# Kernel optimization log

Measured on AMD Instinct MI355X. Metric: run time of the kernel, lower is better.

The kernel has to match this reference:

```python
import jax, jax.numpy as jnp
import numpy as np

FEA, DK, H = 512, 64, 8
B, L = 4, 2048
EPS = 1e-5


def _layernorm(x, g, b):
    mu = jnp.mean(x, axis=-1, keepdims=True)
    var = jnp.mean(jnp.square(x - mu), axis=-1, keepdims=True)
    return (x - mu) * jax.lax.rsqrt(var + EPS) * g + b


def setup_inputs() -> dict:
    key = jax.random.key(0)
    ks = jax.random.split(key, 12)
    d = {
        'qx': jax.random.normal(ks[0], (B, L, FEA), jnp.float32),
        'kx': jax.random.normal(ks[1], (B, L, FEA), jnp.float32),
        'vx': jax.random.normal(ks[2], (B, L, FEA), jnp.float32),
        'maskPAD': jax.random.randint(ks[3], (B, L, L), 0, 2, jnp.int32),
        # attention projections (stored as [in, out]); biases zero-init as in module
        'wq': jax.random.normal(ks[4], (FEA, DK * H), jnp.float32) * 0.02,
        'bq': jnp.zeros((DK * H,), jnp.float32),
        'wk': jax.random.normal(ks[5], (FEA, DK * H), jnp.float32) * 0.02,
        'bk': jnp.zeros((DK * H,), jnp.float32),
        'wv': jax.random.normal(ks[6], (FEA, DK * H), jnp.float32) * 0.02,
        'bv': jnp.zeros((DK * H,), jnp.float32),
        'wo': jax.random.normal(ks[7], (DK * H, FEA), jnp.float32) * 0.02,
        'bo': jnp.zeros((FEA,), jnp.float32),
        # FFN
        'w1': jax.random.normal(ks[8], (FEA, 4 * FEA), jnp.float32) * 0.02,
        'b1': jnp.zeros((4 * FEA,), jnp.float32),
        'w2': jax.random.normal(ks[9], (4 * FEA, FEA), jnp.float32) * 0.02,
        'b2': jnp.zeros((FEA,), jnp.float32),
        # layer norms
        'ln1_g': jnp.ones((FEA,), jnp.float32),
        'ln1_b': jnp.zeros((FEA,), jnp.float32),
        'ln2_g': jnp.ones((FEA,), jnp.float32),
        'ln2_b': jnp.zeros((FEA,), jnp.float32),
    }
    return d


def reference(qx, kx, vx, maskPAD, wq, bq, wk, bk, wv, bv, wo, bo,
              w1, b1, w2, b2, ln1_g, ln1_b, ln2_g, ln2_b):
    b, l, _ = qx.shape
    # project and split heads: [B, H, L, DK]
    q = (qx @ wq + bq).reshape(b, l, H, DK).transpose(0, 2, 1, 3)
    k = (kx @ wk + bk).reshape(b, l, H, DK).transpose(0, 2, 1, 3)
    v = (vx @ wv + bv).reshape(b, l, H, DK).transpose(0, 2, 1, 3)
    scores = jnp.einsum('bhqd,bhkd->bhqk', q, k) / np.sqrt(DK)  # [B,H,L,L]
    mask = (maskPAD == 0)[:, None, :, :]
    scores = jnp.where(mask, jnp.float32(-2 ** 15 + 1), scores)
    alpha = jax.nn.softmax(scores, axis=-1)
    z = jnp.einsum('bhqk,bhkd->bhqd', alpha, v)  # [B,H,L,DK]
    z = z.transpose(0, 2, 1, 3).reshape(b, l, H * DK)
    z = z @ wo + bo
    # post-LN FFN block (dropout = identity at inference)
    zn = _layernorm(vx + z, ln1_g, ln1_b)
    ffn = jax.nn.gelu(zn @ w1 + b1, approximate=False) @ w2 + b2
    return _layernorm(zn + ffn, ln2_g, ln2_b)
```

## Files before the change

kernel.cpp:

```cpp
#include <hip/hip_runtime.h>
#include <cstdint>


typedef __bf16 bf16;
typedef __bf16 bf16x8 __attribute__((ext_vector_type(8)));
typedef __bf16 bf16x2 __attribute__((ext_vector_type(2)));
typedef float floatx4 __attribute__((ext_vector_type(4)));
typedef unsigned uint2v __attribute__((ext_vector_type(2)));

__device__ __forceinline__ floatx4 mfma_bf16(bf16x8 a, bf16x8 b, floatx4 c) {
  return __builtin_amdgcn_mfma_f32_16x16x32_bf16(a, b, c, 0, 0, 0);
}

__device__ __forceinline__ void load_lds_16(const void* g, void* l) {
  auto gp = reinterpret_cast<const void __attribute__((address_space(1)))*>(
      reinterpret_cast<uintptr_t>(g));
  auto lp = reinterpret_cast<void __attribute__((address_space(3)))*>(
      (unsigned int)reinterpret_cast<uintptr_t>(l));
  __builtin_amdgcn_global_load_lds(gp, lp, 16, 0, 0);
}

__device__ __forceinline__ unsigned pack2(float a, float b) {
  bf16x2 p;
  p[0] = (bf16)a;
  p[1] = (bf16)b;
  return __builtin_bit_cast(unsigned, p);
}

__device__ __forceinline__ float gelu_f(float x) {
  float t = 0.7978845608f * (x + 0.044715f * x * x * x);
  float e = __builtin_amdgcn_exp2f(t * 2.885390082f);
  float th = 1.0f - 2.0f * __builtin_amdgcn_rcpf(e + 1.0f);
  return 0.5f * x * (1.0f + th);
}

#define PLANE128 2064
#define PLANE64 1040
#define KVCH 8320

__global__ void __launch_bounds__(256) transpose4_k(const float* __restrict__ w0,
                                                    const float* __restrict__ w1,
                                                    const float* __restrict__ w2,
                                                    const float* __restrict__ w3,
                                                    bf16* __restrict__ o0,
                                                    bf16* __restrict__ o1,
                                                    bf16* __restrict__ o2,
                                                    bf16* __restrict__ o3) {
  const float* in = (blockIdx.z == 0) ? w0 : (blockIdx.z == 1) ? w1
                    : (blockIdx.z == 2) ? w2 : w3;
  bf16* out = (blockIdx.z == 0) ? o0 : (blockIdx.z == 1) ? o1
              : (blockIdx.z == 2) ? o2 : o3;
  __shared__ float tile[32][33];
  int m0 = blockIdx.x * 32, k0 = blockIdx.y * 32;
  int tx = threadIdx.x, ty = threadIdx.y;
  for (int i = ty; i < 32; i += 8)
    tile[i][tx] = in[(size_t)(k0 + i) * 512 + m0 + tx];
  __syncthreads();
  for (int i = ty; i < 32; i += 8)
    out[(size_t)(m0 + i) * 512 + k0 + tx] = (bf16)tile[tx][i];
}

__global__ void __launch_bounds__(256) transpose_k(const float* __restrict__ in,
                                                   bf16* __restrict__ out,
                                                   int K, int M) {
  __shared__ float tile[32][33];
  int m0 = blockIdx.x * 32, k0 = blockIdx.y * 32;
  int tx = threadIdx.x, ty = threadIdx.y;
  for (int i = ty; i < 32; i += 8)
    tile[i][tx] = in[(size_t)(k0 + i) * M + m0 + tx];
  __syncthreads();
  for (int i = ty; i < 32; i += 8)
    out[(size_t)(m0 + i) * K + k0 + tx] = (bf16)tile[tx][i];
}

__global__ void __launch_bounds__(256) maskbits_k(const int* __restrict__ m,
                                                  unsigned long long* __restrict__ out) {
  int w = blockIdx.x * 4 + (threadIdx.x >> 6);
  int lane = threadIdx.x & 63;
  int v = m[(size_t)w * 64 + lane];
  unsigned long long b = __ballot(v != 0);
  if (lane == 0) out[w] = b;
}

template <int EPI>
__device__ __forceinline__ void epi_store(void* Cout, int n, int m, int M,
                                          float val) {
  if constexpr (EPI == 1) {
    int bb = n >> 11, l = n & 2047, hh = m >> 6, d = m & 63;
    ((bf16*)Cout)[((size_t)((bb * 8 + hh) * 2048 + l)) * 64 + d] = (bf16)val;
  } else if constexpr (EPI == 2) {
    int bb = n >> 11, l = n & 2047, hh = m >> 6, d = m & 63;
    ((bf16*)Cout)[((size_t)((bb * 8 + hh) * 64 + d)) * 2048 + l] = (bf16)val;
  } else if constexpr (EPI == 3) {
    ((bf16*)Cout)[(size_t)n * M + m] = (bf16)gelu_f(val);
  } else if constexpr (EPI == 4) {
    ((float*)Cout)[(size_t)n * M + m] = val;
  } else {
    ((float*)Cout)[(size_t)n * M + m] += val;
  }
}

template <int EPI, bool TALL>
__global__ void __launch_bounds__(256) gemm_bt(const bf16* __restrict__ A,
                                               const bf16* __restrict__ Bt,
                                               const float* __restrict__ bias,
                                               void* __restrict__ Cout,
                                               int M, int K, int lda, int ldb) {
  __shared__ __attribute__((aligned(16))) char As[8 * PLANE128];
  __shared__ __attribute__((aligned(16))) char Bs[TALL ? 8 * PLANE64 : 8 * PLANE128];
  int tid = threadIdx.x, wave = tid >> 6, lane = tid & 63;
  int lrow = lane & 15, quad = lane >> 4;
  int n0 = blockIdx.y * 128;
  int m0 = blockIdx.x * (TALL ? 64 : 128);
  int wr = wave >> 1, wc = wave & 1;
  floatx4 zero4 = {0.f, 0.f, 0.f, 0.f};
  constexpr int NI = TALL ? 2 : 4;
  floatx4 acc[NI][4];
#pragma unroll
  for (int i = 0; i < NI; ++i)
#pragma unroll
    for (int j = 0; j < 4; ++j) acc[i][j] = zero4;
  for (int k0 = 0; k0 < K; k0 += 64) {
    __syncthreads();
#pragma unroll
    for (int h = 0; h < 2; ++h) {
      int p = wave + 4 * h;
#pragma unroll
      for (int j = 0; j < 2; ++j) {
        int row = j * 64 + lane;
        load_lds_16(A + (size_t)(n0 + row) * lda + k0 + p * 8,
                    As + p * PLANE128 + j * 1024 + lane * 16);
      }
      if constexpr (TALL) {
        load_lds_16(Bt + (size_t)(m0 + lane) * ldb + k0 + p * 8,
                    Bs + p * PLANE64 + lane * 16);
      } else {
#pragma unroll
        for (int j = 0; j < 2; ++j) {
          int row = j * 64 + lane;
          load_lds_16(Bt + (size_t)(m0 + row) * ldb + k0 + p * 8,
                      Bs + p * PLANE128 + j * 1024 + lane * 16);
        }
      }
    }
    __syncthreads();
#pragma unroll
    for (int h = 0; h < 2; ++h) {
      int pb = h * 4 + quad;
      bf16x8 af[NI], bfr[4];
#pragma unroll
      for (int i = 0; i < NI; ++i) {
        int row = (TALL ? wave * 32 : wr * 64) + i * 16 + lrow;
        af[i] = *(const bf16x8*)(As + pb * PLANE128 + row * 16);
      }
#pragma unroll
      for (int j = 0; j < 4; ++j) {
        if constexpr (TALL)
          bfr[j] = *(const bf16x8*)(Bs + pb * PLANE64 + (j * 16 + lrow) * 16);
        else
          bfr[j] = *(const bf16x8*)(Bs + pb * PLANE128 +
                                    (wc * 64 + j * 16 + lrow) * 16);
      }
#pragma unroll
      for (int i = 0; i < NI; ++i)
#pragma unroll
        for (int j = 0; j < 4; ++j)
          acc[i][j] = mfma_bf16(af[i], bfr[j], acc[i][j]);
    }
  }
  float bv[4];
#pragma unroll
  for (int j = 0; j < 4; ++j) {
    int m = m0 + (TALL ? 0 : wc * 64) + j * 16 + lrow;
    bv[j] = (EPI == 5) ? 0.f : bias[m];
  }
#pragma unroll
  for (int i = 0; i < NI; ++i)
#pragma unroll
    for (int j = 0; j < 4; ++j)
#pragma unroll
      for (int r = 0; r < 4; ++r) {
        int n = n0 + (TALL ? wave * 32 : wr * 64) + i * 16 + quad * 4 + r;
        int m = m0 + (TALL ? 0 : wc * 64) + j * 16 + lrow;
        epi_store<EPI>(Cout, n, m, M, acc[i][j][r] + bv[j]);
      }
}

__global__ void __launch_bounds__(256) qkv_k(const float* __restrict__ qx,
                                             const float* __restrict__ kx,
                                             const float* __restrict__ vx,
                                             const bf16* __restrict__ wqT,
                                             const bf16* __restrict__ wkT,
                                             const bf16* __restrict__ wvT,
                                             const float* __restrict__ bq,
                                             const float* __restrict__ bk,
                                             const float* __restrict__ bv_,
                                             bf16* __restrict__ qh,
                                             bf16* __restrict__ kh,
                                             bf16* __restrict__ vt) {
  __shared__ __attribute__((aligned(16))) char As[8 * PLANE128];
  __shared__ __attribute__((aligned(16))) char Bs[8 * PLANE128];
  int tid = threadIdx.x, wave = tid >> 6, lane = tid & 63;
  int lrow = lane & 15, quad = lane >> 4;
  int seg = blockIdx.y >> 6;
  int n0 = (blockIdx.y & 63) * 128, m0 = blockIdx.x * 128;
  const float* Af = (seg == 0) ? qx : (seg == 1) ? kx : vx;
  const bf16* Bt = (seg == 0) ? wqT : (seg == 1) ? wkT : wvT;
  const float* bias = (seg == 0) ? bq : (seg == 1) ? bk : bv_;
  bf16* out = (seg == 0) ? qh : (seg == 1) ? kh : vt;
  int wr = wave >> 1, wc = wave & 1;
  floatx4 zero4 = {0.f, 0.f, 0.f, 0.f};
  floatx4 acc[4][4];
#pragma unroll
  for (int i = 0; i < 4; ++i)
#pragma unroll
    for (int j = 0; j < 4; ++j) acc[i][j] = zero4;
  int arow = tid >> 2, ap = tid & 3;
  for (int k0 = 0; k0 < 512; k0 += 64) {
    bf16x8 a[4];
#pragma unroll
    for (int u = 0; u < 4; ++u) {
      int row = arow + (u & 1) * 64, p = ap + (u >> 1) * 4;
      const float* src = Af + (size_t)(n0 + row) * 512 + k0 + p * 8;
      float4 x0 = *(const float4*)src;
      float4 x1 = *(const float4*)(src + 4);
      a[u][0] = (bf16)x0.x; a[u][1] = (bf16)x0.y; a[u][2] = (bf16)x0.z;
      a[u][3] = (bf16)x0.w; a[u][4] = (bf16)x1.x; a[u][5] = (bf16)x1.y;
      a[u][6] = (bf16)x1.z; a[u][7] = (bf16)x1.w;
    }
    __syncthreads();
#pragma unroll
    for (int u = 0; u < 4; ++u) {
      int row = arow + (u & 1) * 64, p = ap + (u >> 1) * 4;
      *(bf16x8*)(As + p * PLANE128 + row * 16) = a[u];
    }
#pragma unroll
    for (int h = 0; h < 2; ++h) {
      int p = wave + 4 * h;
#pragma unroll
      for (int j = 0; j < 2; ++j) {
        int row = j * 64 + lane;
        load_lds_16(Bt + (size_t)(m0 + row) * 512 + k0 + p * 8,
                    Bs + p * PLANE128 + j * 1024 + lane * 16);
      }
    }
    __syncthreads();
#pragma unroll
    for (int h = 0; h < 2; ++h) {
      int pb = h * 4 + quad;
      bf16x8 af[4], bfr[4];
#pragma unroll
      for (int t = 0; t < 4; ++t) {
        af[t] = *(const bf16x8*)(As + pb * PLANE128 + (wr * 64 + t * 16 + lrow) * 16);
        bfr[t] = *(const bf16x8*)(Bs + pb * PLANE128 + (wc * 64 + t * 16 + lrow) * 16);
      }
#pragma unroll
      for (int i = 0; i < 4; ++i)
#pragma unroll
        for (int j = 0; j < 4; ++j) acc[i][j] = mfma_bf16(af[i], bfr[j], acc[i][j]);
    }
  }
  float bvv[4];
#pragma unroll
  for (int j = 0; j < 4; ++j) bvv[j] = bias[m0 + wc * 64 + j * 16 + lrow];
  const float qscale = 0.1803368801f;
#pragma unroll
  for (int i = 0; i < 4; ++i)
#pragma unroll
    for (int j = 0; j < 4; ++j)
#pragma unroll
      for (int r = 0; r < 4; ++r) {
        int n = n0 + wr * 64 + i * 16 + quad * 4 + r;
        int m = m0 + wc * 64 + j * 16 + lrow;
        float val = acc[i][j][r] + bvv[j];
        if (seg == 0) val *= qscale;
        int bb = n >> 11, l = n & 2047, hh = m >> 6, d = m & 63;
        if (seg == 2)
          out[((size_t)((bb * 8 + hh) * 64 + d)) * 2048 + l] = (bf16)val;
        else
          out[((size_t)((bb * 8 + hh) * 2048 + l)) * 64 + d] = (bf16)val;
      }
}

__global__ void __launch_bounds__(512, 4) attn_k(const bf16* __restrict__ Qh,
                                                 const bf16* __restrict__ Kh,
                                                 const bf16* __restrict__ Vt,
                                                 const unsigned long long* __restrict__ MB,
                                                 bf16* __restrict__ Z) {
  __shared__ __attribute__((aligned(16))) char smem[8 * KVCH];
  int qt = blockIdx.x, h = blockIdx.y, b = blockIdx.z;
  int tid = threadIdx.x, wave = tid >> 6, lane = tid & 63;
  int hw = wave >> 2, wl = wave & 3;
  int lrow = lane & 15, quad = lane >> 4;
  int q0 = qt * 128;
  size_t headbase = (size_t)(b * 8 + h) * 2048 * 64;

  bf16x8 qf[2][2];
#pragma unroll
  for (int u = 0; u < 2; ++u) {
    const bf16* Qp =
        Qh + headbase + (size_t)(q0 + wl * 32 + u * 16 + lrow) * 64 + quad * 8;
    qf[u][0] = *(const bf16x8*)Qp;
    qf[u][1] = *(const bf16x8*)(Qp + 32);
  }

  floatx4 zero4 = {0.f, 0.f, 0.f, 0.f};
  floatx4 o_acc[2][4], acc_l[2];
#pragma unroll
  for (int u = 0; u < 2; ++u) {
    acc_l[u] = zero4;
#pragma unroll
    for (int dt = 0; dt < 4; ++dt) o_acc[u][dt] = zero4;
  }
  bf16x8 ones;
#pragma unroll
  for (int j = 0; j < 8; ++j) ones[j] = (bf16)1.0f;

  const bf16* Vg = Vt + headbase;
  const bf16* Kg0 = Kh + headbase;
  const uint2* MB0 =
      (const uint2*)(MB + ((size_t)b * 2048 + q0 + wl * 32 + lrow) * 32);
  int sh = quad * 4;

  char* KsH = smem + hw * 2 * KVCH;
  char* VsH = smem + 4 * KVCH + hw * 2 * KVCH;

  auto stage = [&](int buf, int kt) {
    int kk = kt * 64;
    const bf16* Kg = Kg0 + (size_t)kk * 64;
#pragma unroll
    for (int j = 0; j < 2; ++j) {
      int p = wl * 2 + j;
      load_lds_16(Kg + (size_t)lane * 64 + p * 8,
                  KsH + buf * KVCH + p * PLANE64 + lane * 16);
      load_lds_16(Vg + (size_t)lane * 2048 + kk + p * 8,
                  VsH + buf * KVCH + p * PLANE64 + lane * 16);
    }
  };

  int ktbase = hw * 16;
  stage(0, ktbase);
  uint2 mwc[2] = {MB0[ktbase], MB0[512 + ktbase]};

  for (int it = 0; it < 16; ++it) {
    int kt = ktbase + it;
    int cur = it & 1;
    __syncthreads();
    uint2 mwn[2];
    if (it < 15) {
      stage(cur ^ 1, kt + 1);
      mwn[0] = MB0[kt + 1];
      mwn[1] = MB0[512 + kt + 1];
    }
    const char* Kc = KsH + cur * KVCH;
    const char* Vc = VsH + cur * KVCH;
    unsigned S[2][4][2];
#pragma unroll
    for (int nt = 0; nt < 4; ++nt) {
      int R = nt * 16 + lrow;
      bf16x8 k0f = *(const bf16x8*)(Kc + quad * PLANE64 + R * 16);
      bf16x8 k1f = *(const bf16x8*)(Kc + (quad + 4) * PLANE64 + R * 16);
#pragma unroll
      for (int u = 0; u < 2; ++u) {
        floatx4 aa = zero4;
        aa = mfma_bf16(k0f, qf[u][0], aa);
        aa = mfma_bf16(k1f, qf[u][1], aa);
        unsigned wn = ((nt & 2) ? mwc[u].y : mwc[u].x) >> ((nt & 1) * 16 + sh);
        float e[4];
#pragma unroll
        for (int r = 0; r < 4; ++r)
          e[r] = (wn & (1u << r)) ? __builtin_amdgcn_exp2f(aa[r]) : 0.f;
        S[u][nt][0] = pack2(e[0], e[1]);
        S[u][nt][1] = pack2(e[2], e[3]);
      }
    }
    bf16x8 v0[4], v1[4];
#pragma unroll
    for (int dt = 0; dt < 4; ++dt) {
      int R = dt * 16 + lrow;
      v0[dt] = *(const bf16x8*)(Vc + quad * PLANE64 + R * 16);
      v1[dt] = *(const bf16x8*)(Vc + (quad + 4) * PLANE64 + R * 16);
    }
#pragma unroll
    for (int u = 0; u < 2; ++u) {
      union { unsigned w[4]; bf16x8 v; } pf[2];
#pragma unroll
      for (int half = 0; half < 2; ++half)
#pragma unroll
        for (int pr = 0; pr < 2; ++pr) {
          uint2v a = __builtin_amdgcn_permlane32_swap(
              S[u][half * 2][pr], S[u][half * 2 + 1][pr], false, false);
          uint2v c = __builtin_amdgcn_permlane16_swap(a[0], a[1], false, false);
          pf[half].w[pr] = c[0];
          pf[half].w[pr + 2] = c[1];
        }
      bf16x8 pf0 = pf[0].v, pf1 = pf[1].v;
      __builtin_amdgcn_s_setprio(1);
      acc_l[u] = mfma_bf16(pf0, ones, acc_l[u]);
      acc_l[u] = mfma_bf16(pf1, ones, acc_l[u]);
#pragma unroll
      for (int dt = 0; dt < 4; ++dt) {
        o_acc[u][dt] = mfma_bf16(pf0, v0[dt], o_acc[u][dt]);
        o_acc[u][dt] = mfma_bf16(pf1, v1[dt], o_acc[u][dt]);
      }
      __builtin_amdgcn_s_setprio(0);
    }
    if (it < 15) { mwc[0] = mwn[0]; mwc[1] = mwn[1]; }
  }

  __syncthreads();
  float* cb = (float*)smem;
  int cbase = (wl * 64 + lane) * 40;
  if (hw == 1) {
#pragma unroll
    for (int u = 0; u < 2; ++u) {
#pragma unroll
      for (int dt = 0; dt < 4; ++dt)
        *(floatx4*)(cb + cbase + (u * 4 + dt) * 4) = o_acc[u][dt];
      *(floatx4*)(cb + cbase + 32 + u * 4) = acc_l[u];
    }
  }
  __syncthreads();
  if (hw == 0) {
#pragma unroll
    for (int u = 0; u < 2; ++u) {
#pragma unroll
      for (int dt = 0; dt < 4; ++dt)
        o_acc[u][dt] += *(const floatx4*)(cb + cbase + (u * 4 + dt) * 4);
      acc_l[u] += *(const floatx4*)(cb + cbase + 32 + u * 4);
    }
#pragma unroll
    for (int u = 0; u < 2; ++u) {
      float lr[4];
#pragma unroll
      for (int r = 0; r < 4; ++r) lr[r] = 1.0f / acc_l[u][r];
#pragma unroll
      for (int dt = 0; dt < 4; ++dt)
#pragma unroll
        for (int r = 0; r < 4; ++r) {
          int qrow = q0 + wl * 32 + u * 16 + quad * 4 + r;
          int d = dt * 16 + lrow;
          Z[((size_t)(b * 2048 + qrow)) * 512 + h * 64 + d] =
              (bf16)(o_acc[u][dt][r] * lr[r]);
        }
    }
  }
}

template <bool A_BF16, bool OUT_BF16>
__global__ void __launch_bounds__(256) ln_k(const void* __restrict__ a_,
                                            const float* __restrict__ s,
                                            const float* __restrict__ g,
                                            const float* __restrict__ bta,
                                            void* __restrict__ out_) {
  int row = blockIdx.x * 4 + (threadIdx.x >> 6);
  int lane = threadIdx.x & 63;
  size_t base = (size_t)row * 512 + lane * 8;
  float x[8];
  float4 sa = *(const float4*)(s + base);
  float4 sb = *(const float4*)(s + base + 4);
  if constexpr (A_BF16) {
    bf16x8 av = *(const bf16x8*)((const bf16*)a_ + base);
    x[0] = (float)av[0] + sa.x; x[1] = (float)av[1] + sa.y;
    x[2] = (float)av[2] + sa.z; x[3] = (float)av[3] + sa.w;
    x[4] = (float)av[4] + sb.x; x[5] = (float)av[5] + sb.y;
    x[6] = (float)av[6] + sb.z; x[7] = (float)av[7] + sb.w;
  } else {
    float4 a0 = *(const float4*)((const float*)a_ + base);
    float4 a1 = *(const float4*)((const float*)a_ + base + 4);
    x[0] = a0.x + sa.x; x[1] = a0.y + sa.y; x[2] = a0.z + sa.z; x[3] = a0.w + sa.w;
    x[4] = a1.x + sb.x; x[5] = a1.y + sb.y; x[6] = a1.z + sb.z; x[7] = a1.w + sb.w;
  }
  float sum = 0.f;
#pragma unroll
  for (int i = 0; i < 8; ++i) sum += x[i];
#pragma unroll
  for (int off = 1; off < 64; off <<= 1) sum += __shfl_xor(sum, off, 64);
  float mu = sum * (1.0f / 512.0f);
  float vs = 0.f;
#pragma unroll
  for (int i = 0; i < 8; ++i) { float d = x[i] - mu; vs += d * d; }
#pragma unroll
  for (int off = 1; off < 64; off <<= 1) vs += __shfl_xor(vs, off, 64);
  float rstd = rsqrtf(vs * (1.0f / 512.0f) + 1e-5f);
  float4 g0 = *(const float4*)(g + lane * 8);
  float4 g1 = *(const float4*)(g + lane * 8 + 4);
  float4 b0 = *(const float4*)(bta + lane * 8);
  float4 b1 = *(const float4*)(bta + lane * 8 + 4);
  float gg[8] = {g0.x, g0.y, g0.z, g0.w, g1.x, g1.y, g1.z, g1.w};
  float bb[8] = {b0.x, b0.y, b0.z, b0.w, b1.x, b1.y, b1.z, b1.w};
  if constexpr (OUT_BF16) {
    bf16x8 o;
#pragma unroll
    for (int i = 0; i < 8; ++i)
      o[i] = (bf16)((x[i] - mu) * rstd * gg[i] + bb[i]);
    *(bf16x8*)((bf16*)out_ + base) = o;
  } else {
    float4 o0, o1;
    o0.x = (x[0] - mu) * rstd * gg[0] + bb[0];
    o0.y = (x[1] - mu) * rstd * gg[1] + bb[1];
    o0.z = (x[2] - mu) * rstd * gg[2] + bb[2];
    o0.w = (x[3] - mu) * rstd * gg[3] + bb[3];
    o1.x = (x[4] - mu) * rstd * gg[4] + bb[4];
    o1.y = (x[5] - mu) * rstd * gg[5] + bb[5];
    o1.z = (x[6] - mu) * rstd * gg[6] + bb[6];
    o1.w = (x[7] - mu) * rstd * gg[7] + bb[7];
    *(float4*)((float*)out_ + base) = o0;
    *(float4*)((float*)out_ + base + 4) = o1;
  }
}

extern "C" void kernel_launch(void* const* d_in, const int* in_sizes, int n_in,
                              void* d_out, int out_size, void* d_ws, size_t ws_size,
                              hipStream_t stream) {
  const float* qx = (const float*)d_in[0];
  const float* kx = (const float*)d_in[1];
  const float* vx = (const float*)d_in[2];
  const int* maskPAD = (const int*)d_in[3];
  const float* wq = (const float*)d_in[4];
  const float* bq = (const float*)d_in[5];
  const float* wk = (const float*)d_in[6];
  const float* bk = (const float*)d_in[7];
  const float* wv = (const float*)d_in[8];
  const float* bv = (const float*)d_in[9];
  const float* wo = (const float*)d_in[10];
  const float* bo = (const float*)d_in[11];
  const float* w1 = (const float*)d_in[12];
  const float* b1 = (const float*)d_in[13];
  const float* w2 = (const float*)d_in[14];
  const float* b2 = (const float*)d_in[15];
  const float* g1 = (const float*)d_in[16];
  const float* be1 = (const float*)d_in[17];
  const float* g2 = (const float*)d_in[18];
  const float* be2 = (const float*)d_in[19];

  char* w = (char*)d_ws;
  size_t off = 0;
  auto alloc = [&](size_t bytes) {
    void* p = w + off;
    off += (bytes + 255) & ~(size_t)255;
    return p;
  };
  bf16* wqT = (bf16*)alloc(512 * 512 * 2);
  bf16* wkT = (bf16*)alloc(512 * 512 * 2);
  bf16* wvT = (bf16*)alloc(512 * 512 * 2);
  bf16* woT = (bf16*)alloc(512 * 512 * 2);
  bf16* w1T = (bf16*)alloc(2048 * 512 * 2);
  bf16* w2T = (bf16*)alloc(512 * 2048 * 2);
  unsigned long long* mbits = (unsigned long long*)alloc((size_t)4 * 2048 * 32 * 8);
  bf16* qh = (bf16*)alloc((size_t)8192 * 512 * 2);
  bf16* kh = (bf16*)alloc((size_t)8192 * 512 * 2);
  bf16* vt = (bf16*)alloc((size_t)8192 * 512 * 2);
  bf16* z = (bf16*)alloc((size_t)8192 * 512 * 2);
  float* s12 = (float*)qh;
  bf16* zn = vt;
  size_t h1_bytes = (size_t)8192 * 2048 * 2;
  bool big = (off + h1_bytes) <= ws_size;
  bf16* h1 = big ? (bf16*)alloc(h1_bytes) : z;

  dim3 tb(32, 8);
  transpose4_k<<<dim3(16, 16, 4), tb, 0, stream>>>(wq, wk, wv, wo, wqT, wkT, wvT, woT);
  transpose_k<<<dim3(64, 16), tb, 0, stream>>>(w1, w1T, 512, 2048);
  transpose_k<<<dim3(16, 64), tb, 0, stream>>>(w2, w2T, 2048, 512);
  maskbits_k<<<65536, 256, 0, stream>>>(maskPAD, mbits);
  qkv_k<<<dim3(4, 192), 256, 0, stream>>>(qx, kx, vx, wqT, wkT, wvT, bq, bk, bv,
                                          qh, kh, vt);
  attn_k<<<dim3(16, 8, 4), 512, 0, stream>>>(qh, kh, vt, mbits, z);
  gemm_bt<4, true><<<dim3(8, 64), 256, 0, stream>>>(z, woT, bo, s12, 512, 512,
                                                    512, 512);
  ln_k<false, true><<<2048, 256, 0, stream>>>(vx, s12, g1, be1, zn);
  if (big) {
    gemm_bt<3, false><<<dim3(16, 64), 256, 0, stream>>>(zn, w1T, b1, h1, 2048,
                                                        512, 512, 512);
    gemm_bt<4, true><<<dim3(8, 64), 256, 0, stream>>>(h1, w2T, b2, s12, 512,
                                                      2048, 2048, 2048);
  } else {
    for (int p = 0; p < 4; ++p) {
      gemm_bt<3, true><<<dim3(8, 64), 256, 0, stream>>>(
          zn, w1T + (size_t)p * 512 * 512, b1 + p * 512, h1, 512, 512, 512, 512);
      if (p == 0)
        gemm_bt<4, true><<<dim3(8, 64), 256, 0, stream>>>(
            h1, w2T + p * 512, b2, s12, 512, 512, 512, 2048);
      else
        gemm_bt<5, true><<<dim3(8, 64), 256, 0, stream>>>(
            h1, w2T + p * 512, nullptr, s12, 512, 512, 512, 2048);
    }
  }
  ln_k<true, false><<<2048, 256, 0, stream>>>(zn, s12, g2, be2, (float*)d_out);
}
```

Measured before the change: 433.3 us.

## Pre-cast inputs to bf16, tile K/V layouts for contiguous staging, batch maskbits

Adds a separate kernel that casts qx/kx/vx to bf16 so the QKV projection can stage its A operand directly into LDS with async global-to-LDS loads instead of register conversion. The K and V outputs are written in a 64-row tiled, plane-major layout so each attention stage reads contiguous 8 KB tiles rather than strided rows. The mask bitpacking kernel now has each wave process 32 rows, cutting the grid from 65536 blocks to 2048. The trade-off is an extra kernel launch and an extra read/write pass over the inputs.

```diff
diff --git a/kernel.cpp b/kernel.cpp
--- a/kernel.cpp
+++ b/kernel.cpp
@@ -37,6 +37,22 @@
 #define PLANE128 2064
 #define PLANE64 1040
 #define KVCH 8320
+
+__global__ void __launch_bounds__(256) cast3_k(const float* __restrict__ q,
+                                               const float* __restrict__ k,
+                                               const float* __restrict__ v,
+                                               bf16* __restrict__ out) {
+  size_t idx = ((size_t)blockIdx.x * 256 + threadIdx.x) * 8;
+  int sel = (int)(idx >> 22);
+  size_t off = idx & ((1u << 22) - 1);
+  const float* src = (sel == 0) ? q : (sel == 1) ? k : v;
+  float4 a = *(const float4*)(src + off);
+  float4 b = *(const float4*)(src + off + 4);
+  bf16x8 o;
+  o[0] = (bf16)a.x; o[1] = (bf16)a.y; o[2] = (bf16)a.z; o[3] = (bf16)a.w;
+  o[4] = (bf16)b.x; o[5] = (bf16)b.y; o[6] = (bf16)b.z; o[7] = (bf16)b.w;
+  *(bf16x8*)(out + idx) = o;
+}
 
 __global__ void __launch_bounds__(256) transpose4_k(const float* __restrict__ w0,
                                                     const float* __restrict__ w1,
@@ -75,23 +91,21 @@
 
 __global__ void __launch_bounds__(256) maskbits_k(const int* __restrict__ m,
                                                   unsigned long long* __restrict__ out) {
-  int w = blockIdx.x * 4 + (threadIdx.x >> 6);
+  int w0 = blockIdx.x * 128 + (threadIdx.x >> 6) * 32;
   int lane = threadIdx.x & 63;
-  int v = m[(size_t)w * 64 + lane];
-  unsigned long long b = __ballot(v != 0);
-  if (lane == 0) out[w] = b;
+#pragma unroll 4
+  for (int i = 0; i < 32; ++i) {
+    int w = w0 + i;
+    int v = m[(size_t)w * 64 + lane];
+    unsigned long long bmask = __ballot(v != 0);
+    if (lane == 0) out[w] = bmask;
+  }
 }
 
 template <int EPI>
 __device__ __forceinline__ void epi_store(void* Cout, int n, int m, int M,
                                           float val) {
-  if constexpr (EPI == 1) {
-    int bb = n >> 11, l = n & 2047, hh = m >> 6, d = m & 63;
-    ((bf16*)Cout)[((size_t)((bb * 8 + hh) * 2048 + l)) * 64 + d] = (bf16)val;
-  } else if constexpr (EPI == 2) {
-    int bb = n >> 11, l = n & 2047, hh = m >> 6, d = m & 63;
-    ((bf16*)Cout)[((size_t)((bb * 8 + hh) * 64 + d)) * 2048 + l] = (bf16)val;
-  } else if constexpr (EPI == 3) {
+  if constexpr (EPI == 3) {
     ((bf16*)Cout)[(size_t)n * M + m] = (bf16)gelu_f(val);
   } else if constexpr (EPI == 4) {
     ((float*)Cout)[(size_t)n * M + m] = val;
@@ -186,9 +200,7 @@
       }
 }
 
-__global__ void __launch_bounds__(256) qkv_k(const float* __restrict__ qx,
-                                             const float* __restrict__ kx,
-                                             const float* __restrict__ vx,
+__global__ void __launch_bounds__(256) qkv_k(const bf16* __restrict__ xb,
                                              const bf16* __restrict__ wqT,
                                              const bf16* __restrict__ wkT,
                                              const bf16* __restrict__ wvT,
@@ -204,7 +216,7 @@
   int lrow = lane & 15, quad = lane >> 4;
   int seg = blockIdx.y >> 6;
   int n0 = (blockIdx.y & 63) * 128, m0 = blockIdx.x * 128;
-  const float* Af = (seg == 0) ? qx : (seg == 1) ? kx : vx;
+  const bf16* Af = xb + ((size_t)seg << 22);
   const bf16* Bt = (seg == 0) ? wqT : (seg == 1) ? wkT : wvT;
   const float* bias = (seg == 0) ? bq : (seg == 1) ? bk : bv_;
   bf16* out = (seg == 0) ? qh : (seg == 1) ? kh : vt;
@@ -215,31 +227,16 @@
   for (int i = 0; i < 4; ++i)
 #pragma unroll
     for (int j = 0; j < 4; ++j) acc[i][j] = zero4;
-  int arow = tid >> 2, ap = tid & 3;
   for (int k0 = 0; k0 < 512; k0 += 64) {
-    bf16x8 a[4];
-#pragma unroll
-    for (int u = 0; u < 4; ++u) {
-      int row = arow + (u & 1) * 64, p = ap + (u >> 1) * 4;
-      const float* src = Af + (size_t)(n0 + row) * 512 + k0 + p * 8;
-      float4 x0 = *(const float4*)src;
-      float4 x1 = *(const float4*)(src + 4);
-      a[u][0] = (bf16)x0.x; a[u][1] = (bf16)x0.y; a[u][2] = (bf16)x0.z;
-      a[u][3] = (bf16)x0.w; a[u][4] = (bf16)x1.x; a[u][5] = (bf16)x1.y;
-      a[u][6] = (bf16)x1.z; a[u][7] = (bf16)x1.w;
-    }
     __syncthreads();
-#pragma unroll
-    for (int u = 0; u < 4; ++u) {
-      int row = arow + (u & 1) * 64, p = ap + (u >> 1) * 4;
-      *(bf16x8*)(As + p * PLANE128 + row * 16) = a[u];
-    }
 #pragma unroll
     for (int h = 0; h < 2; ++h) {
       int p = wave + 4 * h;
 #pragma unroll
       for (int j = 0; j < 2; ++j) {
         int row = j * 64 + lane;
+        load_lds_16(Af + (size_t)(n0 + row) * 512 + k0 + p * 8,
+                    As + p * PLANE128 + j * 1024 + lane * 16);
         load_lds_16(Bt + (size_t)(m0 + row) * 512 + k0 + p * 8,
                     Bs + p * PLANE128 + j * 1024 + lane * 16);
       }
@@ -273,12 +270,17 @@
         int n = n0 + wr * 64 + i * 16 + quad * 4 + r;
         int m = m0 + wc * 64 + j * 16 + lrow;
         float val = acc[i][j][r] + bvv[j];
-        if (seg == 0) val *= qscale;
         int bb = n >> 11, l = n & 2047, hh = m >> 6, d = m & 63;
-        if (seg == 2)
-          out[((size_t)((bb * 8 + hh) * 64 + d)) * 2048 + l] = (bf16)val;
-        else
-          out[((size_t)((bb * 8 + hh) * 2048 + l)) * 64 + d] = (bf16)val;
+        if (seg == 0) {
+          out[((size_t)((bb * 8 + hh) * 2048 + l)) * 64 + d] =
+              (bf16)(val * qscale);
+        } else {
+          size_t tb_ = ((size_t)((bb * 8 + hh) * 32 + (l >> 6))) * 4096;
+          if (seg == 1)
+            out[tb_ + (d >> 3) * 512 + (l & 63) * 8 + (d & 7)] = (bf16)val;
+          else
+            out[tb_ + ((l >> 3) & 7) * 512 + d * 8 + (l & 7)] = (bf16)val;
+        }
       }
 }
 
@@ -316,8 +318,8 @@
 #pragma unroll
   for (int j = 0; j < 8; ++j) ones[j] = (bf16)1.0f;
 
-  const bf16* Vg = Vt + headbase;
-  const bf16* Kg0 = Kh + headbase;
+  const bf16* Kt0 = Kh + headbase;
+  const bf16* Vt0 = Vt + headbase;
   const uint2* MB0 =
       (const uint2*)(MB + ((size_t)b * 2048 + q0 + wl * 32 + lrow) * 32);
   int sh = quad * 4;
@@ -326,14 +328,14 @@
   char* VsH = smem + 4 * KVCH + hw * 2 * KVCH;
 
   auto stage = [&](int buf, int kt) {
-    int kk = kt * 64;
-    const bf16* Kg = Kg0 + (size_t)kk * 64;
+    const bf16* Ktile = Kt0 + (size_t)kt * 4096;
+    const bf16* Vtile = Vt0 + (size_t)kt * 4096;
 #pragma unroll
     for (int j = 0; j < 2; ++j) {
       int p = wl * 2 + j;
-      load_lds_16(Kg + (size_t)lane * 64 + p * 8,
+      load_lds_16(Ktile + p * 512 + lane * 8,
                   KsH + buf * KVCH + p * PLANE64 + lane * 16);
-      load_lds_16(Vg + (size_t)lane * 2048 + kk + p * 8,
+      load_lds_16(Vtile + p * 512 + lane * 8,
                   VsH + buf * KVCH + p * PLANE64 + lane * 16);
     }
   };
@@ -548,6 +550,7 @@
   bf16* w1T = (bf16*)alloc(2048 * 512 * 2);
   bf16* w2T = (bf16*)alloc(512 * 2048 * 2);
   unsigned long long* mbits = (unsigned long long*)alloc((size_t)4 * 2048 * 32 * 8);
+  bf16* xb = (bf16*)alloc((size_t)3 * 4194304 * 2);
   bf16* qh = (bf16*)alloc((size_t)8192 * 512 * 2);
   bf16* kh = (bf16*)alloc((size_t)8192 * 512 * 2);
   bf16* vt = (bf16*)alloc((size_t)8192 * 512 * 2);
@@ -562,8 +565,9 @@
   transpose4_k<<<dim3(16, 16, 4), tb, 0, stream>>>(wq, wk, wv, wo, wqT, wkT, wvT, woT);
   transpose_k<<<dim3(64, 16), tb, 0, stream>>>(w1, w1T, 512, 2048);
   transpose_k<<<dim3(16, 64), tb, 0, stream>>>(w2, w2T, 2048, 512);
-  maskbits_k<<<65536, 256, 0, stream>>>(maskPAD, mbits);
-  qkv_k<<<dim3(4, 192), 256, 0, stream>>>(qx, kx, vx, wqT, wkT, wvT, bq, bk, bv,
+  maskbits_k<<<2048, 256, 0, stream>>>(maskPAD, mbits);
+  cast3_k<<<6144, 256, 0, stream>>>(qx, kx, vx, xb);
+  qkv_k<<<dim3(4, 192), 256, 0, stream>>>(xb, wqT, wkT, wvT, bq, bk, bv,
                                           qh, kh, vt);
   attn_k<<<dim3(16, 8, 4), 512, 0, stream>>>(qh, kh, vt, mbits, z);
   gemm_bt<4, true><<<dim3(8, 64), 256, 0, stream>>>(z, woT, bo, s12, 512, 512,
```

After: 426.2 us. Within noise of the previous version (-1.7%).
